# Optimization experiments

Hardware: AMD Instinct MI355X
Metric: run time of the kernel (lower is better)

Reference implementation:

```python
import jax, jax.numpy as jnp
import numpy as np

EPS = 1e-5


def setup_inputs() -> dict:
    key = jax.random.key(0)
    k1, k2 = jax.random.split(key, 2)
    B, L, C = 2, 385, 128  # L = N+1 tokens (CLS at index 0), N = 384
    x = jax.random.normal(k1, (B, L, C), dtype=jnp.float32)
    gamma = jnp.ones((1, 1, 1, 2 * C), dtype=jnp.float32)
    beta = jnp.zeros((1, 1, 1, 2 * C), dtype=jnp.float32)
    W = jax.random.normal(k2, (C, 2 * C), dtype=jnp.float32) / np.float32(np.sqrt(2 * C))
    b = jnp.zeros((C,), dtype=jnp.float32)
    return {"x": x, "gamma": gamma, "beta": beta, "W": W, "b": b}


def reference(x, gamma, beta, W, b):
    cls_tok = x[:, :1, :]                 # [B,1,C]
    F = x[:, 1:, :]                       # [B,N,C]
    # diff[b,i,j,:] = F[b,j] - F[b,i]  (center i on axis 1, neighbor j on axis 2)
    diff = F[:, None, :, :] - F[:, :, None, :]            # [B,N,N,C]
    var = jnp.var(diff, axis=2, keepdims=True)            # biased var over neighbors, [B,N,1,C]
    F_tilde = diff / jnp.sqrt(var + EPS)                  # [B,N,N,C]
    F_center = jnp.broadcast_to(F[:, :, None, :], diff.shape)
    Fc_K = jnp.concatenate([F_tilde, F_center], axis=-1) * gamma + beta  # [B,N,N,2C]
    weights = jax.nn.softmax(Fc_K, axis=2)                # softmax over neighbors
    Fc_C = jnp.sum(weights * Fc_K, axis=2)                # [B,N,2C]
    tokens = Fc_C @ W.T + b                               # align: Linear(2C -> C)
    return jnp.concatenate([cls_tok, tokens], axis=1)     # [B,L,C]
```

## Files before the change

kernel.cpp:

```cpp
#include <hip/hip_runtime.h>
#include <hip/hip_bf16.h>
#include <math.h>


#define B_  2
#define L_  385
#define C_  128
#define N_  384
#define EPS_ 1e-5f
#define MROWS_ 32
#define RB_  (N_ / MROWS_)
#define NTHR_ 1024
#define LOG2E_ 1.44269504088896340736f

typedef short short8 __attribute__((ext_vector_type(8)));
typedef float f32x4 __attribute__((ext_vector_type(4)));

union V16 { ushort us[8]; uint4 v4; };

__device__ inline ushort f2bf(float f) {
  __hip_bfloat16 hb = __float2bfloat16(f);
  return __builtin_bit_cast(ushort, hb);
}

__device__ inline float fast_exp2(float xv) {
#if __has_builtin(__builtin_amdgcn_exp2f)
  return __builtin_amdgcn_exp2f(xv);
#else
  float r;
  asm("v_exp_f32 %0, %1" : "=v"(r) : "v"(xv));
  return r;
#endif
}

__global__ __launch_bounds__(NTHR_, 1) void lnp_kernel(
    const float* __restrict__ x, const float* __restrict__ gamma,
    const float* __restrict__ beta, const float* __restrict__ W,
    const float* __restrict__ bvec, float* __restrict__ out) {
  __shared__ __align__(16) float p1[32][128];
  __shared__ __align__(16) float p2[32][128];
  __shared__ __align__(16) float sA[128], slA[128], shA[128];
  __shared__ __align__(16) float facL[256];
  __shared__ __align__(16) ushort Wb[128 * 256];
  __shared__ __align__(16) ushort As[MROWS_ * 256];

  const int blk = blockIdx.x;
  const int b   = blk / RB_;
  const int rt  = blk % RB_;
  const int r0  = rt * MROWS_;
  const int t   = threadIdx.x;

  const float* Fb = x + (size_t)b * (L_ * C_) + C_;

  if (rt == 0 && t < C_)
    out[(size_t)b * (L_ * C_) + t] = x[(size_t)b * (L_ * C_) + t];

  const int tc = t & 31;
  const int c4 = tc * 4;
  const int h  = t >> 5;
  float4 v[12];
  {
    const float* p = Fb + (size_t)(h * 12) * C_ + c4;
#pragma unroll
    for (int r = 0; r < 12; ++r)
      v[r] = *(const float4*)(p + (size_t)r * C_);

    float ax = 0.f, ay = 0.f, az = 0.f, aw = 0.f;
    float qx = 0.f, qy = 0.f, qz = 0.f, qw = 0.f;
#pragma unroll
    for (int r = 0; r < 12; ++r) {
      ax += v[r].x; qx = fmaf(v[r].x, v[r].x, qx);
      ay += v[r].y; qy = fmaf(v[r].y, v[r].y, qy);
      az += v[r].z; qz = fmaf(v[r].z, v[r].z, qz);
      aw += v[r].w; qw = fmaf(v[r].w, v[r].w, qw);
    }
    float4 s1 = {ax, ay, az, aw};
    float4 s2 = {qx, qy, qz, qw};
    *(float4*)&p1[h][c4] = s1;
    *(float4*)&p2[h][c4] = s2;
  }
  {
    const int c  = t >> 3;
    const int kb = (t & 7) * 32;
    const int swz = (c & 7) << 3;
#pragma unroll
    for (int q = 0; q < 4; ++q) {
      const int kk = kb + q * 8;
      const float* wp = &W[c * 256 + kk];
      const float4 wa  = *(const float4*)wp;
      const float4 wb2 = *(const float4*)(wp + 4);
      V16 pk;
      pk.us[0] = f2bf(wa.x);  pk.us[1] = f2bf(wa.y);
      pk.us[2] = f2bf(wa.z);  pk.us[3] = f2bf(wa.w);
      pk.us[4] = f2bf(wb2.x); pk.us[5] = f2bf(wb2.y);
      pk.us[6] = f2bf(wb2.z); pk.us[7] = f2bf(wb2.w);
      *(uint4*)&Wb[c * 256 + (kk ^ swz)] = pk.v4;
    }
  }
  __syncthreads();

  if (t < 128) {
    float s1 = 0.f, s2 = 0.f;
#pragma unroll
    for (int g = 0; g < 32; ++g) { s1 += p1[g][t]; s2 += p2[g][t]; }
    const float mean = s1 * (1.0f / N_);
    const float var  = fmaxf(s2 * (1.0f / N_) - mean * mean, 0.0f);
    const float s    = gamma[t] * rsqrtf(var + EPS_);
    const float sl   = s * LOG2E_;
    sA[t] = s; slA[t] = sl; shA[t] = sl * mean;
    facL[128 + t] = beta[128 + t];
  }
  __syncthreads();

  {
    const float4 sl4 = *(const float4*)&slA[c4];
    const float4 sh4 = *(const float4*)&shA[c4];
    float ex = 0.f, ey = 0.f, ez = 0.f, ew = 0.f;
    float fx = 0.f, fy = 0.f, fz = 0.f, fw = 0.f;
#pragma unroll
    for (int r = 0; r < 12; ++r) {
      const float e0 = fast_exp2(fmaf(sl4.x, v[r].x, -sh4.x));
      const float e1 = fast_exp2(fmaf(sl4.y, v[r].y, -sh4.y));
      const float e2 = fast_exp2(fmaf(sl4.z, v[r].z, -sh4.z));
      const float e3 = fast_exp2(fmaf(sl4.w, v[r].w, -sh4.w));
      ex += e0; fx = fmaf(e0, v[r].x, fx);
      ey += e1; fy = fmaf(e1, v[r].y, fy);
      ez += e2; fz = fmaf(e2, v[r].z, fz);
      ew += e3; fw = fmaf(e3, v[r].w, fw);
    }
    float4 se = {ex, ey, ez, ew};
    float4 sf = {fx, fy, fz, fw};
    *(float4*)&p1[h][c4] = se;
    *(float4*)&p2[h][c4] = sf;
  }

  const int ai  = t >> 5;
  const int kk0 = (t & 31) * 8;
  const int ks  = kk0 & 127;
  float4 af0, af1, g40 = {0,0,0,0}, g41 = {0,0,0,0};
  {
    const float* fp = &Fb[(size_t)(r0 + ai) * C_ + ks];
    af0 = *(const float4*)fp;
    af1 = *(const float4*)(fp + 4);
    if (kk0 >= 128) {
      g40 = *(const float4*)&gamma[kk0];
      g41 = *(const float4*)&gamma[kk0 + 4];
    }
  }
  __syncthreads();

  const int aswz_w = (ai & 7) << 3;
  if (kk0 >= 128) {
    const float4 fc0 = *(const float4*)&facL[kk0];
    const float4 fc1 = *(const float4*)&facL[kk0 + 4];
    V16 pk;
    pk.us[0] = f2bf(fmaf(g40.x, af0.x, fc0.x));
    pk.us[1] = f2bf(fmaf(g40.y, af0.y, fc0.y));
    pk.us[2] = f2bf(fmaf(g40.z, af0.z, fc0.z));
    pk.us[3] = f2bf(fmaf(g40.w, af0.w, fc0.w));
    pk.us[4] = f2bf(fmaf(g41.x, af1.x, fc1.x));
    pk.us[5] = f2bf(fmaf(g41.y, af1.y, fc1.y));
    pk.us[6] = f2bf(fmaf(g41.z, af1.z, fc1.z));
    pk.us[7] = f2bf(fmaf(g41.w, af1.w, fc1.w));
    *(uint4*)&As[ai * 256 + (kk0 ^ aswz_w)] = pk.v4;
  }
  if (t < 128) {
    float se = 0.f, sf = 0.f;
#pragma unroll
    for (int g = 0; g < 32; ++g) { se += p1[g][t]; sf += p2[g][t]; }
    facL[t] = fmaf(sA[t], sf / se, beta[t]);
  }
  __syncthreads();

  if (kk0 < 128) {
    const float4 sa0 = *(const float4*)&sA[kk0];
    const float4 sa1 = *(const float4*)&sA[kk0 + 4];
    const float4 fc0 = *(const float4*)&facL[kk0];
    const float4 fc1 = *(const float4*)&facL[kk0 + 4];
    V16 pk;
    pk.us[0] = f2bf(fmaf(-sa0.x, af0.x, fc0.x));
    pk.us[1] = f2bf(fmaf(-sa0.y, af0.y, fc0.y));
    pk.us[2] = f2bf(fmaf(-sa0.z, af0.z, fc0.z));
    pk.us[3] = f2bf(fmaf(-sa0.w, af0.w, fc0.w));
    pk.us[4] = f2bf(fmaf(-sa1.x, af1.x, fc1.x));
    pk.us[5] = f2bf(fmaf(-sa1.y, af1.y, fc1.y));
    pk.us[6] = f2bf(fmaf(-sa1.z, af1.z, fc1.z));
    pk.us[7] = f2bf(fmaf(-sa1.w, af1.w, fc1.w));
    *(uint4*)&As[ai * 256 + (kk0 ^ aswz_w)] = pk.v4;
  }
  __syncthreads();

  {
    const int w   = t >> 6;
    const int l   = t & 63;
    const int tn  = w & 7;
    const int tm  = w >> 3;
    const int l16 = l & 15;
    const int lg  = l >> 4;

    const int ar = tm * 16 + l16;
    const int bc = tn * 16 + l16;
    const int abase = ar * 256;
    const int bbase = bc * 256;
    const int aswz = (ar & 7) << 3;
    const int bswz = (bc & 7) << 3;

    f32x4 acc = {0.f, 0.f, 0.f, 0.f};
#pragma unroll
    for (int kt = 0; kt < 8; ++kt) {
      const int kk = kt * 32 + lg * 8;
      const short8 av = *(const short8*)&As[abase + (kk ^ aswz)];
      const short8 bv = *(const short8*)&Wb[bbase + (kk ^ bswz)];
      acc = __builtin_amdgcn_mfma_f32_16x16x32_bf16(av, bv, acc, 0, 0, 0);
    }

    const float bb = bvec[bc];
    float* ob = out + (size_t)b * (L_ * C_);
#pragma unroll
    for (int r = 0; r < 4; ++r) {
      const int m = tm * 16 + lg * 4 + r;
      ob[(size_t)(1 + r0 + m) * C_ + bc] = acc[r] + bb;
    }
  }
}

extern "C" void kernel_launch(void* const* d_in, const int* in_sizes, int n_in,
                              void* d_out, int out_size, void* d_ws, size_t ws_size,
                              hipStream_t stream) {
  const float* x     = (const float*)d_in[0];
  const float* gamma = (const float*)d_in[1];
  const float* beta  = (const float*)d_in[2];
  const float* W     = (const float*)d_in[3];
  const float* bvec  = (const float*)d_in[4];
  float* out = (float*)d_out;

  lnp_kernel<<<B_ * RB_, NTHR_, 0, stream>>>(x, gamma, beta, W, bvec, out);
}
```

Baseline: 15.02 us.

## Split into prep kernel for per-batch stats and bf16 W, then lean GEMM kernel

Before, each of the 24 blocks recomputed the per-channel statistics for its whole batch and converted all of W to bf16 in shared memory. Now a small prep kernel computes the per-batch scale and softmax factor once, writes bf16 W to workspace, and copies the CLS rows. The main kernel only builds its A tile and loads its W fragments straight into registers. This removes redundant reductions and syncs from the main kernel, but adds a second kernel launch and a global-memory round trip through workspace.

Result: slower. 15.83 us (+5.4%).

```diff
diff --git a/kernel.cpp b/kernel.cpp
--- a/kernel.cpp
+++ b/kernel.cpp
@@ -7,16 +7,17 @@
 #define L_  385
 #define C_  128
 #define N_  384
+#define LC_ (L_ * C_)
 #define EPS_ 1e-5f
 #define MROWS_ 32
 #define RB_  (N_ / MROWS_)
-#define NTHR_ 1024
 #define LOG2E_ 1.44269504088896340736f
 
 typedef short short8 __attribute__((ext_vector_type(8)));
 typedef float f32x4 __attribute__((ext_vector_type(4)));
 
 union V16 { ushort us[8]; uint4 v4; };
+union U16 { uint4 v4; short8 s8; };
 
 __device__ inline ushort f2bf(float f) {
   __hip_bfloat16 hb = __float2bfloat16(f);
@@ -33,31 +34,40 @@
 #endif
 }
 
-__global__ __launch_bounds__(NTHR_, 1) void lnp_kernel(
+__global__ __launch_bounds__(1024, 1) void lnp_prep(
     const float* __restrict__ x, const float* __restrict__ gamma,
     const float* __restrict__ beta, const float* __restrict__ W,
-    const float* __restrict__ bvec, float* __restrict__ out) {
-  __shared__ __align__(16) float p1[32][128];
-  __shared__ __align__(16) float p2[32][128];
-  __shared__ __align__(16) float sA[128], slA[128], shA[128];
-  __shared__ __align__(16) float facL[256];
-  __shared__ __align__(16) ushort Wb[128 * 256];
-  __shared__ __align__(16) ushort As[MROWS_ * 256];
-
+    float* __restrict__ wsNegS, float* __restrict__ wsFac,
+    ushort* __restrict__ wsWbf, float* __restrict__ out) {
   const int blk = blockIdx.x;
-  const int b   = blk / RB_;
-  const int rt  = blk % RB_;
-  const int r0  = rt * MROWS_;
   const int t   = threadIdx.x;
 
-  const float* Fb = x + (size_t)b * (L_ * C_) + C_;
-
-  if (rt == 0 && t < C_)
-    out[(size_t)b * (L_ * C_) + t] = x[(size_t)b * (L_ * C_) + t];
-
+  if (blk >= 2) {
+    const int base = (blk - 2) * 8192 + t * 8;
+    const float4 wa  = *(const float4*)&W[base];
+    const float4 wb2 = *(const float4*)&W[base + 4];
+    V16 pk;
+    pk.us[0] = f2bf(wa.x);  pk.us[1] = f2bf(wa.y);
+    pk.us[2] = f2bf(wa.z);  pk.us[3] = f2bf(wa.w);
+    pk.us[4] = f2bf(wb2.x); pk.us[5] = f2bf(wb2.y);
+    pk.us[6] = f2bf(wb2.z); pk.us[7] = f2bf(wb2.w);
+    *(uint4*)&wsWbf[base] = pk.v4;
+    if (blk == 2 && t < C_) out[t] = x[t];
+    if (blk == 3 && t < C_) out[LC_ + t] = x[LC_ + t];
+    return;
+  }
+
+  __shared__ __align__(16) float p1[16][128], p2[16][128];
+  __shared__ float sA[128], slA[128], shA[128];
+
+  const int b  = blk;
+  const float* Fb = x + (size_t)b * LC_ + C_;
   const int tc = t & 31;
   const int c4 = tc * 4;
   const int h  = t >> 5;
+  const int w  = t >> 6;
+  const int l  = t & 63;
+
   float4 v[12];
   {
     const float* p = Fb + (size_t)(h * 12) * C_ + c4;
@@ -74,27 +84,15 @@
       az += v[r].z; qz = fmaf(v[r].z, v[r].z, qz);
       aw += v[r].w; qw = fmaf(v[r].w, v[r].w, qw);
     }
-    float4 s1 = {ax, ay, az, aw};
-    float4 s2 = {qx, qy, qz, qw};
-    *(float4*)&p1[h][c4] = s1;
-    *(float4*)&p2[h][c4] = s2;
-  }
-  {
-    const int c  = t >> 3;
-    const int kb = (t & 7) * 32;
-    const int swz = (c & 7) << 3;
-#pragma unroll
-    for (int q = 0; q < 4; ++q) {
-      const int kk = kb + q * 8;
-      const float* wp = &W[c * 256 + kk];
-      const float4 wa  = *(const float4*)wp;
-      const float4 wb2 = *(const float4*)(wp + 4);
-      V16 pk;
-      pk.us[0] = f2bf(wa.x);  pk.us[1] = f2bf(wa.y);
-      pk.us[2] = f2bf(wa.z);  pk.us[3] = f2bf(wa.w);
-      pk.us[4] = f2bf(wb2.x); pk.us[5] = f2bf(wb2.y);
-      pk.us[6] = f2bf(wb2.z); pk.us[7] = f2bf(wb2.w);
-      *(uint4*)&Wb[c * 256 + (kk ^ swz)] = pk.v4;
+    ax += __shfl_xor(ax, 32); ay += __shfl_xor(ay, 32);
+    az += __shfl_xor(az, 32); aw += __shfl_xor(aw, 32);
+    qx += __shfl_xor(qx, 32); qy += __shfl_xor(qy, 32);
+    qz += __shfl_xor(qz, 32); qw += __shfl_xor(qw, 32);
+    if (l < 32) {
+      float4 s1 = {ax, ay, az, aw};
+      float4 s2 = {qx, qy, qz, qw};
+      *(float4*)&p1[w][c4] = s1;
+      *(float4*)&p2[w][c4] = s2;
     }
   }
   __syncthreads();
@@ -102,13 +100,13 @@
   if (t < 128) {
     float s1 = 0.f, s2 = 0.f;
 #pragma unroll
-    for (int g = 0; g < 32; ++g) { s1 += p1[g][t]; s2 += p2[g][t]; }
+    for (int g = 0; g < 16; ++g) { s1 += p1[g][t]; s2 += p2[g][t]; }
     const float mean = s1 * (1.0f / N_);
     const float var  = fmaxf(s2 * (1.0f / N_) - mean * mean, 0.0f);
     const float s    = gamma[t] * rsqrtf(var + EPS_);
     const float sl   = s * LOG2E_;
     sA[t] = s; slA[t] = sl; shA[t] = sl * mean;
-    facL[128 + t] = beta[128 + t];
+    wsNegS[b * 128 + t] = -s;
   }
   __syncthreads();
 
@@ -128,94 +126,93 @@
       ez += e2; fz = fmaf(e2, v[r].z, fz);
       ew += e3; fw = fmaf(e3, v[r].w, fw);
     }
-    float4 se = {ex, ey, ez, ew};
-    float4 sf = {fx, fy, fz, fw};
-    *(float4*)&p1[h][c4] = se;
-    *(float4*)&p2[h][c4] = sf;
-  }
+    ex += __shfl_xor(ex, 32); ey += __shfl_xor(ey, 32);
+    ez += __shfl_xor(ez, 32); ew += __shfl_xor(ew, 32);
+    fx += __shfl_xor(fx, 32); fy += __shfl_xor(fy, 32);
+    fz += __shfl_xor(fz, 32); fw += __shfl_xor(fw, 32);
+    if (l < 32) {
+      float4 se = {ex, ey, ez, ew};
+      float4 sf = {fx, fy, fz, fw};
+      *(float4*)&p1[w][c4] = se;
+      *(float4*)&p2[w][c4] = sf;
+    }
+  }
+  __syncthreads();
+
+  if (t < 128) {
+    float se = 0.f, sf = 0.f;
+#pragma unroll
+    for (int g = 0; g < 16; ++g) { se += p1[g][t]; sf += p2[g][t]; }
+    wsFac[b * 128 + t] = fmaf(sA[t], sf / se, beta[t]);
+  }
+}
+
+__global__ __launch_bounds__(1024, 1) void lnp_main(
+    const float* __restrict__ x, const float* __restrict__ gamma,
+    const float* __restrict__ beta, const float* __restrict__ bvec,
+    const float* __restrict__ wsNegS, const float* __restrict__ wsFac,
+    const ushort* __restrict__ wsWbf, float* __restrict__ out) {
+  __shared__ __align__(16) ushort As[MROWS_ * 256];
+
+  const int blk = blockIdx.x;
+  const int b   = blk / RB_;
+  const int rt  = blk % RB_;
+  const int r0  = rt * MROWS_;
+  const int t   = threadIdx.x;
+  const int wv  = t >> 6;
+  const int l   = t & 63;
+  const int l16 = l & 15;
+  const int lg  = l >> 4;
+  const int tn  = wv & 7;
+  const int tm  = wv >> 3;
+  const int bc  = tn * 16 + l16;
+  const int ar  = tm * 16 + l16;
 
   const int ai  = t >> 5;
   const int kk0 = (t & 31) * 8;
   const int ks  = kk0 & 127;
-  float4 af0, af1, g40 = {0,0,0,0}, g41 = {0,0,0,0};
-  {
-    const float* fp = &Fb[(size_t)(r0 + ai) * C_ + ks];
-    af0 = *(const float4*)fp;
-    af1 = *(const float4*)(fp + 4);
-    if (kk0 >= 128) {
-      g40 = *(const float4*)&gamma[kk0];
-      g41 = *(const float4*)&gamma[kk0 + 4];
-    }
-  }
-  __syncthreads();
-
-  const int aswz_w = (ai & 7) << 3;
-  if (kk0 >= 128) {
-    const float4 fc0 = *(const float4*)&facL[kk0];
-    const float4 fc1 = *(const float4*)&facL[kk0 + 4];
+  const float* fp = x + (size_t)b * LC_ + C_ + (size_t)(r0 + ai) * C_ + ks;
+  const float4 af0 = *(const float4*)fp;
+  const float4 af1 = *(const float4*)(fp + 4);
+  const float* pA = (kk0 < 128) ? (wsNegS + b * 128 + kk0) : (gamma + kk0);
+  const float* pB = (kk0 < 128) ? (wsFac + b * 128 + kk0) : (beta + kk0);
+  const float4 cA0 = *(const float4*)pA;
+  const float4 cA1 = *(const float4*)(pA + 4);
+  const float4 cB0 = *(const float4*)pB;
+  const float4 cB1 = *(const float4*)(pB + 4);
+
+  U16 wb[8];
+  const ushort* wrow = wsWbf + bc * 256 + lg * 8;
+#pragma unroll
+  for (int kt = 0; kt < 8; ++kt)
+    wb[kt].v4 = *(const uint4*)(wrow + kt * 32);
+  const float bb = bvec[bc];
+
+  {
     V16 pk;
-    pk.us[0] = f2bf(fmaf(g40.x, af0.x, fc0.x));
-    pk.us[1] = f2bf(fmaf(g40.y, af0.y, fc0.y));
-    pk.us[2] = f2bf(fmaf(g40.z, af0.z, fc0.z));
-    pk.us[3] = f2bf(fmaf(g40.w, af0.w, fc0.w));
-    pk.us[4] = f2bf(fmaf(g41.x, af1.x, fc1.x));
-    pk.us[5] = f2bf(fmaf(g41.y, af1.y, fc1.y));
-    pk.us[6] = f2bf(fmaf(g41.z, af1.z, fc1.z));
-    pk.us[7] = f2bf(fmaf(g41.w, af1.w, fc1.w));
-    *(uint4*)&As[ai * 256 + (kk0 ^ aswz_w)] = pk.v4;
-  }
-  if (t < 128) {
-    float se = 0.f, sf = 0.f;
-#pragma unroll
-    for (int g = 0; g < 32; ++g) { se += p1[g][t]; sf += p2[g][t]; }
-    facL[t] = fmaf(sA[t], sf / se, beta[t]);
-  }
-  __syncthreads();
-
-  if (kk0 < 128) {
-    const float4 sa0 = *(const float4*)&sA[kk0];
-    const float4 sa1 = *(const float4*)&sA[kk0 + 4];
-    const float4 fc0 = *(const float4*)&facL[kk0];
-    const float4 fc1 = *(const float4*)&facL[kk0 + 4];
-    V16 pk;
-    pk.us[0] = f2bf(fmaf(-sa0.x, af0.x, fc0.x));
-    pk.us[1] = f2bf(fmaf(-sa0.y, af0.y, fc0.y));
-    pk.us[2] = f2bf(fmaf(-sa0.z, af0.z, fc0.z));
-    pk.us[3] = f2bf(fmaf(-sa0.w, af0.w, fc0.w));
-    pk.us[4] = f2bf(fmaf(-sa1.x, af1.x, fc1.x));
-    pk.us[5] = f2bf(fmaf(-sa1.y, af1.y, fc1.y));
-    pk.us[6] = f2bf(fmaf(-sa1.z, af1.z, fc1.z));
-    pk.us[7] = f2bf(fmaf(-sa1.w, af1.w, fc1.w));
-    *(uint4*)&As[ai * 256 + (kk0 ^ aswz_w)] = pk.v4;
-  }
-  __syncthreads();
-
-  {
-    const int w   = t >> 6;
-    const int l   = t & 63;
-    const int tn  = w & 7;
-    const int tm  = w >> 3;
-    const int l16 = l & 15;
-    const int lg  = l >> 4;
-
-    const int ar = tm * 16 + l16;
-    const int bc = tn * 16 + l16;
+    pk.us[0] = f2bf(fmaf(cA0.x, af0.x, cB0.x));
+    pk.us[1] = f2bf(fmaf(cA0.y, af0.y, cB0.y));
+    pk.us[2] = f2bf(fmaf(cA0.z, af0.z, cB0.z));
+    pk.us[3] = f2bf(fmaf(cA0.w, af0.w, cB0.w));
+    pk.us[4] = f2bf(fmaf(cA1.x, af1.x, cB1.x));
+    pk.us[5] = f2bf(fmaf(cA1.y, af1.y, cB1.y));
+    pk.us[6] = f2bf(fmaf(cA1.z, af1.z, cB1.z));
+    pk.us[7] = f2bf(fmaf(cA1.w, af1.w, cB1.w));
+    *(uint4*)&As[ai * 256 + (kk0 ^ ((ai & 7) << 3))] = pk.v4;
+  }
+  __syncthreads();
+
+  {
     const int abase = ar * 256;
-    const int bbase = bc * 256;
-    const int aswz = (ar & 7) << 3;
-    const int bswz = (bc & 7) << 3;
-
+    const int aswz  = (ar & 7) << 3;
     f32x4 acc = {0.f, 0.f, 0.f, 0.f};
 #pragma unroll
     for (int kt = 0; kt < 8; ++kt) {
       const int kk = kt * 32 + lg * 8;
       const short8 av = *(const short8*)&As[abase + (kk ^ aswz)];
-      const short8 bv = *(const short8*)&Wb[bbase + (kk ^ bswz)];
-      acc = __builtin_amdgcn_mfma_f32_16x16x32_bf16(av, bv, acc, 0, 0, 0);
-    }
-
-    const float bb = bvec[bc];
-    float* ob = out + (size_t)b * (L_ * C_);
+      acc = __builtin_amdgcn_mfma_f32_16x16x32_bf16(av, wb[kt].s8, acc, 0, 0, 0);
+    }
+    float* ob = out + (size_t)b * LC_;
 #pragma unroll
     for (int r = 0; r < 4; ++r) {
       const int m = tm * 16 + lg * 4 + r;
@@ -234,5 +231,11 @@
   const float* bvec  = (const float*)d_in[4];
   float* out = (float*)d_out;
 
-  lnp_kernel<<<B_ * RB_, NTHR_, 0, stream>>>(x, gamma, beta, W, bvec, out);
-}
+  float*  wsNegS = (float*)d_ws;
+  float*  wsFac  = wsNegS + 256;
+  ushort* wsWbf  = (ushort*)(wsNegS + 512);
+
+  lnp_prep<<<6, 1024, 0, stream>>>(x, gamma, beta, W, wsNegS, wsFac, wsWbf, out);
+  lnp_main<<<B_ * RB_, 1024, 0, stream>>>(x, gamma, beta, bvec,
+                                          wsNegS, wsFac, wsWbf, out);
+}
```
